# Kernel tuning notes

Hardware: AMD Instinct MI355X
Metric: run time of the kernel (lower is better)

Reference implementation:

```python
import jax, jax.numpy as jnp
import numpy as np

B, S, H = 64, 2048, 256
H3 = 3 * H


def setup_inputs() -> dict:
    key = jax.random.key(0)
    ks = jax.random.split(key, 5)
    static = jax.random.normal(ks[0], (B, S, H), dtype=jnp.float32)
    dynamic = jax.random.normal(ks[1], (B, S, H), dtype=jnp.float32)
    decoder_hidden = jax.random.normal(ks[2], (B, H), dtype=jnp.float32)
    # learned params (nn.Parameter in original); scale ~ 1/sqrt(fan_in)
    v = jax.random.normal(ks[3], (1, H3), dtype=jnp.float32) / np.sqrt(H3)
    W = jax.random.normal(ks[4], (H3, H3), dtype=jnp.float32) / np.sqrt(H3)
    return {"static": static, "dynamic": dynamic,
            "decoder_hidden": decoder_hidden, "v": v, "W": W}


def reference(static, dynamic, decoder_hidden, v, W):
    # cat = concat(static[i,j], dynamic[i,j], decoder_hidden[i]) -> [B, S, 3H]
    dec = jnp.broadcast_to(decoder_hidden[:, None, :], static.shape)
    cat = jnp.concatenate([static, dynamic, dec], axis=-1)
    # score[b,s] = v . tanh(W @ cat[b,s])
    hidden = jnp.tanh(jnp.einsum('ok,bsk->bso', W, cat))  # [B, S, 3H]
    scores = jnp.einsum('bso,o->bs', hidden, v[0])        # [B, S]
    return jax.nn.softmax(scores, axis=1)
```

## Files before the change

### kernel.cpp

```cpp
#include <hip/hip_runtime.h>
#include <hip/hip_bf16.h>

#define B_   64
#define S_   2048
#define H_   256
#define H3_  768
#define K_   512
#define MT   64
#define RSTR 1040

typedef __attribute__((ext_vector_type(8))) short  bf16x8;
typedef __attribute__((ext_vector_type(4))) float  f32x4;

__device__ __forceinline__ uint pkbf2(float a, float b) {
    float2 f = make_float2(a, b);
    __hip_bfloat162 h = __float22bfloat162_rn(f);
    return *reinterpret_cast<uint*>(&h);
}

__global__ void pack_w(const float* __restrict__ W, short* __restrict__ wpk) {
    int t = blockIdx.x * 256 + threadIdx.x;
    if (t >= 48 * 16 * 64) return;
    int lane = t & 63;
    int ks   = (t >> 6) & 15;
    int ot   = t >> 10;
    int o  = ot * 16 + (lane & 15);
    int kb = ks * 32 + (lane >> 4) * 8;
    const float* src = W + (size_t)o * H3_ + kb;
    float4 a = ((const float4*)src)[0];
    float4 b = ((const float4*)src)[1];
    uint4 pk;
    pk.x = pkbf2(a.x, a.y);
    pk.y = pkbf2(a.z, a.w);
    pk.z = pkbf2(b.x, b.y);
    pk.w = pkbf2(b.z, b.w);
    *(uint4*)(wpk + (size_t)t * 8) = pk;
}

__global__ void bias_k(const float* __restrict__ W, const float* __restrict__ dec,
                       const float* __restrict__ v, float* __restrict__ bias,
                       float* __restrict__ vsum) {
    if (blockIdx.x == 192) {
        if (threadIdx.x < 64) {
            float s = 0.f;
#pragma unroll
            for (int i = 0; i < 12; ++i) s += v[threadIdx.x + i * 64];
#pragma unroll
            for (int off = 32; off >= 1; off >>= 1) s += __shfl_xor(s, off);
            if (threadIdx.x == 0) vsum[0] = s;
        }
        return;
    }
    int idx = blockIdx.x * 256 + threadIdx.x;
    int b = idx / H3_;
    int o = idx - b * H3_;
    const float4* wr = (const float4*)(W + (size_t)o * H3_ + 2 * H_);
    const float4* dv = (const float4*)(dec + (size_t)b * H_);
    float s = 0.f;
#pragma unroll 8
    for (int k = 0; k < H_ / 4; ++k) {
        float4 a = wr[k], d = dv[k];
        s += a.x * d.x + a.y * d.y + a.z * d.z + a.w * d.w;
    }
    bias[idx] = s;
}

__global__ __launch_bounds__(512, 2)
void score_k(const float* __restrict__ stat, const float* __restrict__ dyn,
             const short* __restrict__ wpk, const float* __restrict__ bias,
             const float* __restrict__ v, const float* __restrict__ vsum,
             float* __restrict__ scores) {
    __shared__ char  aT[MT * RSTR];
    __shared__ float sred[8][MT];

    const int tid  = threadIdx.x;
    const int pos0 = blockIdx.x * MT;
    const int bidx = pos0 >> 11;

    const int wave = tid >> 6;
    const int lane = tid & 63;
    const int lr = lane & 15;
    const int lg = lane >> 4;

    const short* wbase = wpk + (size_t)lane * 8;

    bf16x8 bcur[3];
#pragma unroll
    for (int ni = 0; ni < 3; ++ni)
        bcur[ni] = *(const bf16x8*)(wbase + (size_t)(wave * 6 + ni) * 8192);

    {
        const int kcol = lane * 8;
        const float* srcbase = (kcol < 256) ? (stat + kcol) : (dyn + (kcol - 256));
#pragma unroll
        for (int bat = 0; bat < 2; ++bat) {
            float4 f0[4], f1[4];
#pragma unroll
            for (int u = 0; u < 4; ++u) {
                int row = (bat * 4 + u) * 8 + wave;
                const float4* p = (const float4*)(srcbase + (size_t)(pos0 + row) * H_);
                f0[u] = p[0];
                f1[u] = p[1];
            }
#pragma unroll
            for (int u = 0; u < 4; ++u) {
                int row = (bat * 4 + u) * 8 + wave;
                uint4 pk;
                pk.x = pkbf2(f0[u].x, f0[u].y);
                pk.y = pkbf2(f0[u].z, f0[u].w);
                pk.z = pkbf2(f1[u].x, f1[u].y);
                pk.w = pkbf2(f1[u].z, f1[u].w);
                *(uint4*)(aT + row * RSTR + lane * 16) = pk;
            }
        }
    }
    __syncthreads();

    const char* abase = aT + lr * RSTR + lg * 16;

    float sacc[4][4];
#pragma unroll
    for (int mi = 0; mi < 4; ++mi)
#pragma unroll
        for (int j = 0; j < 4; ++j) sacc[mi][j] = 0.f;

    const float C1 = 2.8853900817779268f;

#pragma unroll
    for (int p = 0; p < 2; ++p) {
        const int obase = wave * 96 + p * 48;

        float bv[3], vv2[3];
#pragma unroll
        for (int ni = 0; ni < 3; ++ni) {
            int o = obase + ni * 16 + lr;
            bv[ni]  = bias[bidx * H3_ + o];
            vv2[ni] = -2.0f * v[o];
        }

        f32x4 acc[4][3];
#pragma unroll
        for (int mi = 0; mi < 4; ++mi)
#pragma unroll
            for (int ni = 0; ni < 3; ++ni) {
                f32x4 a = {bv[ni], bv[ni], bv[ni], bv[ni]};
                acc[mi][ni] = a;
            }

        const short* wp0 = wbase + (size_t)(wave * 6 + p * 3) * 8192;

#pragma unroll 4
        for (int ks = 0; ks < 16; ++ks) {
            const int ksn = (ks + 1) & 15;
            bf16x8 bnx[3];
#pragma unroll
            for (int ni = 0; ni < 3; ++ni)
                bnx[ni] = *(const bf16x8*)(wp0 + ni * 8192 + ksn * 512);
            bf16x8 afr[4];
#pragma unroll
            for (int mi = 0; mi < 4; ++mi)
                afr[mi] = *(const bf16x8*)(abase + mi * 16 * RSTR + ks * 64);
            __builtin_amdgcn_s_setprio(1);
#pragma unroll
            for (int mi = 0; mi < 4; ++mi)
#pragma unroll
                for (int ni = 0; ni < 3; ++ni)
                    acc[mi][ni] = __builtin_amdgcn_mfma_f32_16x16x32_bf16(
                        afr[mi], bcur[ni], acc[mi][ni], 0, 0, 0);
            __builtin_amdgcn_s_setprio(0);
#pragma unroll
            for (int ni = 0; ni < 3; ++ni) bcur[ni] = bnx[ni];
        }

        if (p == 0) {
            const short* wpn = wbase + (size_t)(wave * 6 + 3) * 8192;
#pragma unroll
            for (int ni = 0; ni < 3; ++ni)
                bcur[ni] = *(const bf16x8*)(wpn + ni * 8192);
        }

#pragma unroll
        for (int ni = 0; ni < 3; ++ni)
#pragma unroll
            for (int mi = 0; mi < 4; ++mi)
#pragma unroll
                for (int j = 0; j < 4; ++j) {
                    float e = __builtin_amdgcn_exp2f(acc[mi][ni][j] * C1);
                    float r = __builtin_amdgcn_rcpf(e + 1.0f);
                    sacc[mi][j] = fmaf(vv2[ni], r, sacc[mi][j]);
                }
    }

#pragma unroll
    for (int mi = 0; mi < 4; ++mi)
#pragma unroll
        for (int j = 0; j < 4; ++j) {
            float x = sacc[mi][j];
            x += __shfl_xor(x, 1);
            x += __shfl_xor(x, 2);
            x += __shfl_xor(x, 4);
            x += __shfl_xor(x, 8);
            sacc[mi][j] = x;
        }
    if (lr == 0) {
#pragma unroll
        for (int mi = 0; mi < 4; ++mi)
#pragma unroll
            for (int j = 0; j < 4; ++j)
                sred[wave][mi * 16 + lg * 4 + j] = sacc[mi][j];
    }
    __syncthreads();
    if (tid < MT) {
        float s = vsum[0];
#pragma unroll
        for (int w = 0; w < 8; ++w) s += sred[w][tid];
        scores[pos0 + tid] = s;
    }
}

__global__ void softmax_k(float* __restrict__ out) {
    const int b = blockIdx.x;
    float* row = out + (size_t)b * S_;
    const int tid  = threadIdx.x;
    const int wave = tid >> 6;
    const int lane = tid & 63;

    float vals[8];
    float m = -1e30f;
#pragma unroll
    for (int i = 0; i < 8; ++i) {
        vals[i] = row[tid + i * 256];
        m = fmaxf(m, vals[i]);
    }
#pragma unroll
    for (int off = 32; off >= 1; off >>= 1) m = fmaxf(m, __shfl_xor(m, off));
    __shared__ float redm[4];
    __shared__ float reds[4];
    if (lane == 0) redm[wave] = m;
    __syncthreads();
    m = fmaxf(fmaxf(redm[0], redm[1]), fmaxf(redm[2], redm[3]));

    float s = 0.f;
#pragma unroll
    for (int i = 0; i < 8; ++i) {
        vals[i] = __expf(vals[i] - m);
        s += vals[i];
    }
#pragma unroll
    for (int off = 32; off >= 1; off >>= 1) s += __shfl_xor(s, off);
    if (lane == 0) reds[wave] = s;
    __syncthreads();
    s = reds[0] + reds[1] + reds[2] + reds[3];
    float inv = 1.0f / s;
#pragma unroll
    for (int i = 0; i < 8; ++i) row[tid + i * 256] = vals[i] * inv;
}

extern "C" void kernel_launch(void* const* d_in, const int* in_sizes, int n_in,
                              void* d_out, int out_size, void* d_ws, size_t ws_size,
                              hipStream_t stream) {
    const float* stat = (const float*)d_in[0];
    const float* dyn  = (const float*)d_in[1];
    const float* dec  = (const float*)d_in[2];
    const float* v    = (const float*)d_in[3];
    const float* W    = (const float*)d_in[4];
    float* out = (float*)d_out;

    short* wpk  = (short*)d_ws;
    float* bias = (float*)((char*)d_ws + (size_t)H3_ * K_ * 2);
    float* vsum = bias + B_ * H3_;

    pack_w <<<(48 * 16 * 64 + 255) / 256, 256, 0, stream>>>(W, wpk);
    bias_k <<<193, 256, 0, stream>>>(W, dec, v, bias, vsum);
    score_k<<<(B_ * S_) / MT, 512, 0, stream>>>(stat, dyn, wpk, bias, v, vsum, out);
    softmax_k<<<B_, 256, 0, stream>>>(out);
}
```

Measured before the change: 158.1 us.

## Split output columns across four blocks per tile with double-buffered K staging

Each 64-row tile is now processed by four 256-thread blocks, each owning a quarter of the output columns. Activations are staged in 128-column chunks into double-buffered LDS, so global loads overlap with MFMA work. Weights are loaded directly per k-step. Partial scores go to a workspace that softmax sums, and the constant v-sum term is dropped because softmax is shift-invariant. The change raises occupancy and overlap at the cost of reading each activation tile four times from global or L2 memory.

```diff
diff --git a/kernel.cpp b/kernel.cpp
--- a/kernel.cpp
+++ b/kernel.cpp
@@ -7,7 +7,7 @@
 #define H3_  768
 #define K_   512
 #define MT   64
-#define RSTR 1040
+#define RST  136
 
 typedef __attribute__((ext_vector_type(8))) short  bf16x8;
 typedef __attribute__((ext_vector_type(4))) float  f32x4;
@@ -38,20 +38,9 @@
 }
 
 __global__ void bias_k(const float* __restrict__ W, const float* __restrict__ dec,
-                       const float* __restrict__ v, float* __restrict__ bias,
-                       float* __restrict__ vsum) {
-    if (blockIdx.x == 192) {
-        if (threadIdx.x < 64) {
-            float s = 0.f;
-#pragma unroll
-            for (int i = 0; i < 12; ++i) s += v[threadIdx.x + i * 64];
-#pragma unroll
-            for (int off = 32; off >= 1; off >>= 1) s += __shfl_xor(s, off);
-            if (threadIdx.x == 0) vsum[0] = s;
-        }
-        return;
-    }
+                       float* __restrict__ bias) {
     int idx = blockIdx.x * 256 + threadIdx.x;
+    if (idx >= B_ * H3_) return;
     int b = idx / H3_;
     int o = idx - b * H3_;
     const float4* wr = (const float4*)(W + (size_t)o * H3_ + 2 * H_);
@@ -65,131 +54,119 @@
     bias[idx] = s;
 }
 
-__global__ __launch_bounds__(512, 2)
+__global__ __launch_bounds__(256, 4)
 void score_k(const float* __restrict__ stat, const float* __restrict__ dyn,
              const short* __restrict__ wpk, const float* __restrict__ bias,
-             const float* __restrict__ v, const float* __restrict__ vsum,
-             float* __restrict__ scores) {
-    __shared__ char  aT[MT * RSTR];
-    __shared__ float sred[8][MT];
+             const float* __restrict__ v, float* __restrict__ part) {
+    __shared__ short aT[2][MT * RST];
+    __shared__ float sred[4][MT];
 
     const int tid  = threadIdx.x;
-    const int pos0 = blockIdx.x * MT;
+    const int bid  = blockIdx.x;
+    const int rt   = bid >> 2;
+    const int g    = bid & 3;
+    const int pos0 = rt * MT;
     const int bidx = pos0 >> 11;
 
     const int wave = tid >> 6;
     const int lane = tid & 63;
-    const int lr = lane & 15;
-    const int lg = lane >> 4;
-
-    const short* wbase = wpk + (size_t)lane * 8;
-
-    bf16x8 bcur[3];
-#pragma unroll
-    for (int ni = 0; ni < 3; ++ni)
-        bcur[ni] = *(const bf16x8*)(wbase + (size_t)(wave * 6 + ni) * 8192);
-
-    {
-        const int kcol = lane * 8;
-        const float* srcbase = (kcol < 256) ? (stat + kcol) : (dyn + (kcol - 256));
-#pragma unroll
-        for (int bat = 0; bat < 2; ++bat) {
-            float4 f0[4], f1[4];
-#pragma unroll
-            for (int u = 0; u < 4; ++u) {
-                int row = (bat * 4 + u) * 8 + wave;
-                const float4* p = (const float4*)(srcbase + (size_t)(pos0 + row) * H_);
-                f0[u] = p[0];
-                f1[u] = p[1];
-            }
-#pragma unroll
-            for (int u = 0; u < 4; ++u) {
-                int row = (bat * 4 + u) * 8 + wave;
-                uint4 pk;
-                pk.x = pkbf2(f0[u].x, f0[u].y);
-                pk.y = pkbf2(f0[u].z, f0[u].w);
-                pk.z = pkbf2(f1[u].x, f1[u].y);
-                pk.w = pkbf2(f1[u].z, f1[u].w);
-                *(uint4*)(aT + row * RSTR + lane * 16) = pk;
-            }
-        }
-    }
-    __syncthreads();
-
-    const char* abase = aT + lr * RSTR + lg * 16;
-
-    float sacc[4][4];
+    const int lr   = lane & 15;
+    const int lg   = lane >> 4;
+
+    const float C1 = 2.8853900817779268f;
+
+    float bv[3], vv2[3];
+#pragma unroll
+    for (int ni = 0; ni < 3; ++ni) {
+        int o = (g * 12 + wave * 3 + ni) * 16 + lr;
+        bv[ni]  = bias[bidx * H3_ + o];
+        vv2[ni] = -2.0f * v[o];
+    }
+
+    const int srow = tid >> 2;
+    const int q    = tid & 3;
+    float4 f0[4], f1[4];
+    auto stage_load = [&](int ch) {
+        const float* base = (ch < 2)
+            ? (stat + (size_t)(pos0 + srow) * H_ + ch * 128 + q * 32)
+            : (dyn  + (size_t)(pos0 + srow) * H_ + (ch - 2) * 128 + q * 32);
+#pragma unroll
+        for (int u = 0; u < 4; ++u) {
+            f0[u] = ((const float4*)base)[u * 2];
+            f1[u] = ((const float4*)base)[u * 2 + 1];
+        }
+    };
+    auto stage_write = [&](int bufi) {
+        short* dst = aT[bufi] + srow * RST + q * 32;
+#pragma unroll
+        for (int u = 0; u < 4; ++u) {
+            uint4 pk;
+            pk.x = pkbf2(f0[u].x, f0[u].y);
+            pk.y = pkbf2(f0[u].z, f0[u].w);
+            pk.z = pkbf2(f1[u].x, f1[u].y);
+            pk.w = pkbf2(f1[u].z, f1[u].w);
+            *(uint4*)(dst + u * 8) = pk;
+        }
+    };
+
+    f32x4 acc[4][3];
 #pragma unroll
     for (int mi = 0; mi < 4; ++mi)
 #pragma unroll
-        for (int j = 0; j < 4; ++j) sacc[mi][j] = 0.f;
-
-    const float C1 = 2.8853900817779268f;
-
-#pragma unroll
-    for (int p = 0; p < 2; ++p) {
-        const int obase = wave * 96 + p * 48;
-
-        float bv[3], vv2[3];
-#pragma unroll
         for (int ni = 0; ni < 3; ++ni) {
-            int o = obase + ni * 16 + lr;
-            bv[ni]  = bias[bidx * H3_ + o];
-            vv2[ni] = -2.0f * v[o];
-        }
-
-        f32x4 acc[4][3];
-#pragma unroll
-        for (int mi = 0; mi < 4; ++mi)
-#pragma unroll
-            for (int ni = 0; ni < 3; ++ni) {
-                f32x4 a = {bv[ni], bv[ni], bv[ni], bv[ni]};
-                acc[mi][ni] = a;
-            }
-
-        const short* wp0 = wbase + (size_t)(wave * 6 + p * 3) * 8192;
-
-#pragma unroll 4
-        for (int ks = 0; ks < 16; ++ks) {
-            const int ksn = (ks + 1) & 15;
-            bf16x8 bnx[3];
+            f32x4 a = {bv[ni], bv[ni], bv[ni], bv[ni]};
+            acc[mi][ni] = a;
+        }
+
+    const short* wbase = wpk + (size_t)(g * 12 + wave * 3) * 8192 + lane * 8;
+
+    stage_load(0);
+    stage_write(0);
+    __syncthreads();
+
+#pragma unroll 1
+    for (int ch = 0; ch < 4; ++ch) {
+        if (ch < 3) stage_load(ch + 1);
+        const short* abuf = aT[ch & 1] + lr * RST + lg * 8;
+#pragma unroll
+        for (int ksl = 0; ksl < 4; ++ksl) {
+            const int ks = ch * 4 + ksl;
+            bf16x8 bfr[3];
 #pragma unroll
             for (int ni = 0; ni < 3; ++ni)
-                bnx[ni] = *(const bf16x8*)(wp0 + ni * 8192 + ksn * 512);
+                bfr[ni] = *(const bf16x8*)(wbase + ni * 8192 + ks * 512);
             bf16x8 afr[4];
 #pragma unroll
             for (int mi = 0; mi < 4; ++mi)
-                afr[mi] = *(const bf16x8*)(abase + mi * 16 * RSTR + ks * 64);
+                afr[mi] = *(const bf16x8*)(abuf + mi * 16 * RST + ksl * 32);
             __builtin_amdgcn_s_setprio(1);
 #pragma unroll
             for (int mi = 0; mi < 4; ++mi)
 #pragma unroll
                 for (int ni = 0; ni < 3; ++ni)
                     acc[mi][ni] = __builtin_amdgcn_mfma_f32_16x16x32_bf16(
-                        afr[mi], bcur[ni], acc[mi][ni], 0, 0, 0);
+                        afr[mi], bfr[ni], acc[mi][ni], 0, 0, 0);
             __builtin_amdgcn_s_setprio(0);
-#pragma unroll
-            for (int ni = 0; ni < 3; ++ni) bcur[ni] = bnx[ni];
-        }
-
-        if (p == 0) {
-            const short* wpn = wbase + (size_t)(wave * 6 + 3) * 8192;
-#pragma unroll
-            for (int ni = 0; ni < 3; ++ni)
-                bcur[ni] = *(const bf16x8*)(wpn + ni * 8192);
-        }
-
-#pragma unroll
-        for (int ni = 0; ni < 3; ++ni)
-#pragma unroll
-            for (int mi = 0; mi < 4; ++mi)
-#pragma unroll
-                for (int j = 0; j < 4; ++j) {
-                    float e = __builtin_amdgcn_exp2f(acc[mi][ni][j] * C1);
-                    float r = __builtin_amdgcn_rcpf(e + 1.0f);
-                    sacc[mi][j] = fmaf(vv2[ni], r, sacc[mi][j]);
-                }
-    }
+        }
+        if (ch < 3) stage_write((ch + 1) & 1);
+        __syncthreads();
+    }
+
+    float sacc[4][4];
+#pragma unroll
+    for (int mi = 0; mi < 4; ++mi)
+#pragma unroll
+        for (int j = 0; j < 4; ++j) sacc[mi][j] = 0.f;
+#pragma unroll
+    for (int ni = 0; ni < 3; ++ni)
+#pragma unroll
+        for (int mi = 0; mi < 4; ++mi)
+#pragma unroll
+            for (int j = 0; j < 4; ++j) {
+                float e = __builtin_amdgcn_exp2f(acc[mi][ni][j] * C1);
+                float r = __builtin_amdgcn_rcpf(e + 1.0f);
+                sacc[mi][j] = fmaf(vv2[ni], r, sacc[mi][j]);
+            }
 
 #pragma unroll
     for (int mi = 0; mi < 4; ++mi)
@@ -211,25 +188,25 @@
     }
     __syncthreads();
     if (tid < MT) {
-        float s = vsum[0];
-#pragma unroll
-        for (int w = 0; w < 8; ++w) s += sred[w][tid];
-        scores[pos0 + tid] = s;
-    }
-}
-
-__global__ void softmax_k(float* __restrict__ out) {
+        float s = sred[0][tid] + sred[1][tid] + sred[2][tid] + sred[3][tid];
+        part[(size_t)g * (B_ * S_) + pos0 + tid] = s;
+    }
+}
+
+__global__ void softmax_k(const float* __restrict__ part, float* __restrict__ out) {
     const int b = blockIdx.x;
-    float* row = out + (size_t)b * S_;
     const int tid  = threadIdx.x;
     const int wave = tid >> 6;
     const int lane = tid & 63;
+    const int base = b * S_;
 
     float vals[8];
     float m = -1e30f;
 #pragma unroll
     for (int i = 0; i < 8; ++i) {
-        vals[i] = row[tid + i * 256];
+        int idx = base + tid + i * 256;
+        vals[i] = part[idx] + part[idx + B_ * S_] + part[idx + 2 * B_ * S_]
+                + part[idx + 3 * B_ * S_];
         m = fmaxf(m, vals[i]);
     }
 #pragma unroll
@@ -252,6 +229,7 @@
     __syncthreads();
     s = reds[0] + reds[1] + reds[2] + reds[3];
     float inv = 1.0f / s;
+    float* row = out + (size_t)base;
 #pragma unroll
     for (int i = 0; i < 8; ++i) row[tid + i * 256] = vals[i] * inv;
 }
@@ -268,10 +246,10 @@
 
     short* wpk  = (short*)d_ws;
     float* bias = (float*)((char*)d_ws + (size_t)H3_ * K_ * 2);
-    float* vsum = bias + B_ * H3_;
+    float* part = bias + B_ * H3_;
 
     pack_w <<<(48 * 16 * 64 + 255) / 256, 256, 0, stream>>>(W, wpk);
-    bias_k <<<193, 256, 0, stream>>>(W, dec, v, bias, vsum);
-    score_k<<<(B_ * S_) / MT, 512, 0, stream>>>(stat, dyn, wpk, bias, v, vsum, out);
-    softmax_k<<<B_, 256, 0, stream>>>(out);
-}
+    bias_k <<<(B_ * H3_ + 255) / 256, 256, 0, stream>>>(W, dec, bias);
+    score_k<<<(B_ * S_ / MT) * 4, 256, 0, stream>>>(stat, dyn, wpk, bias, v, part);
+    softmax_k<<<B_, 256, 0, stream>>>(part, out);
+}
```

Result: slower. 590.5 us (+273.4%).

## Double M tile to 128 rows and overlap dynamic-half loads with MFMA

Applied to the files above, without the earlier changes.

The score kernel tile grows from 64 to 128 positions per block, so each weight fragment loaded from global memory feeds twice as many MFMAs. The static and dynamic halves of the activation tile are staged separately, and the dynamic half's global loads and bf16 packing are interleaved with the first eight k-steps of the first output pass, hiding part of the load latency. The softmax-invariant vsum constant is dropped, and launch bounds fall to one block per SM. The larger register and LDS footprint lowers occupancy and spills could hurt.

```diff
diff --git a/kernel.cpp b/kernel.cpp
--- a/kernel.cpp
+++ b/kernel.cpp
@@ -5,9 +5,9 @@
 #define S_   2048
 #define H_   256
 #define H3_  768
-#define K_   512
-#define MT   64
-#define RSTR 1040
+#define MT   128
+#define RSH  528
+#define HALF (MT * RSH)
 
 typedef __attribute__((ext_vector_type(8))) short  bf16x8;
 typedef __attribute__((ext_vector_type(4))) float  f32x4;
@@ -38,20 +38,9 @@
 }
 
 __global__ void bias_k(const float* __restrict__ W, const float* __restrict__ dec,
-                       const float* __restrict__ v, float* __restrict__ bias,
-                       float* __restrict__ vsum) {
-    if (blockIdx.x == 192) {
-        if (threadIdx.x < 64) {
-            float s = 0.f;
-#pragma unroll
-            for (int i = 0; i < 12; ++i) s += v[threadIdx.x + i * 64];
-#pragma unroll
-            for (int off = 32; off >= 1; off >>= 1) s += __shfl_xor(s, off);
-            if (threadIdx.x == 0) vsum[0] = s;
-        }
-        return;
-    }
+                       float* __restrict__ bias) {
     int idx = blockIdx.x * 256 + threadIdx.x;
+    if (idx >= B_ * H3_) return;
     int b = idx / H3_;
     int o = idx - b * H3_;
     const float4* wr = (const float4*)(W + (size_t)o * H3_ + 2 * H_);
@@ -65,12 +54,11 @@
     bias[idx] = s;
 }
 
-__global__ __launch_bounds__(512, 2)
+__global__ __launch_bounds__(512, 1)
 void score_k(const float* __restrict__ stat, const float* __restrict__ dyn,
              const short* __restrict__ wpk, const float* __restrict__ bias,
-             const float* __restrict__ v, const float* __restrict__ vsum,
-             float* __restrict__ scores) {
-    __shared__ char  aT[MT * RSTR];
+             const float* __restrict__ v, float* __restrict__ scores) {
+    __shared__ char  aT[2 * HALF];
     __shared__ float sred[8][MT];
 
     const int tid  = threadIdx.x;
@@ -79,110 +67,120 @@
 
     const int wave = tid >> 6;
     const int lane = tid & 63;
-    const int lr = lane & 15;
-    const int lg = lane >> 4;
-
+    const int lr   = lane & 15;
+    const int lg   = lane >> 4;
+
+    const float C1 = 2.8853900817779268f;
     const short* wbase = wpk + (size_t)lane * 8;
 
+    float4 f0[4], f1[4];
+    auto loadb = [&](int h, int bat) {
+        const float* srcb = (h == 0) ? stat : dyn;
+#pragma unroll
+        for (int i = 0; i < 4; ++i) {
+            int lin = (bat * 4 + i) * 512 + tid;
+            int row = lin >> 5;
+            int un  = lin & 31;
+            const float4* p = (const float4*)(srcb + (size_t)(pos0 + row) * H_ + un * 8);
+            f0[i] = p[0];
+            f1[i] = p[1];
+        }
+    };
+    auto writeb = [&](int h, int bat) {
+#pragma unroll
+        for (int i = 0; i < 4; ++i) {
+            int lin = (bat * 4 + i) * 512 + tid;
+            int row = lin >> 5;
+            int un  = lin & 31;
+            uint4 pk;
+            pk.x = pkbf2(f0[i].x, f0[i].y);
+            pk.y = pkbf2(f0[i].z, f0[i].w);
+            pk.z = pkbf2(f1[i].x, f1[i].y);
+            pk.w = pkbf2(f1[i].z, f1[i].w);
+            *(uint4*)(aT + h * HALF + row * RSH + un * 16) = pk;
+        }
+    };
+
+    loadb(0, 0); writeb(0, 0);
+    loadb(0, 1); writeb(0, 1);
+    __syncthreads();
+
+    float sacc[8][4];
+#pragma unroll
+    for (int mi = 0; mi < 8; ++mi)
+#pragma unroll
+        for (int j = 0; j < 4; ++j) sacc[mi][j] = 0.f;
+
+    const char* abase0 = aT + lr * RSH + lg * 16;
+
+    f32x4 acc[8][3];
     bf16x8 bcur[3];
-#pragma unroll
-    for (int ni = 0; ni < 3; ++ni)
-        bcur[ni] = *(const bf16x8*)(wbase + (size_t)(wave * 6 + ni) * 8192);
+    auto ksstep = [&](const short* wp, int ks) {
+        const int h = ks >> 3, ksl = ks & 7;
+        const int ksn = (ks + 1) & 15;
+        bf16x8 bnx[3];
+#pragma unroll
+        for (int ni = 0; ni < 3; ++ni)
+            bnx[ni] = *(const bf16x8*)(wp + ni * 8192 + ksn * 512);
+        const char* ab = abase0 + h * HALF + ksl * 64;
+        bf16x8 afr[8];
+#pragma unroll
+        for (int mi = 0; mi < 8; ++mi)
+            afr[mi] = *(const bf16x8*)(ab + mi * (16 * RSH));
+        __builtin_amdgcn_s_setprio(1);
+#pragma unroll
+        for (int mi = 0; mi < 8; ++mi)
+#pragma unroll
+            for (int ni = 0; ni < 3; ++ni)
+                acc[mi][ni] = __builtin_amdgcn_mfma_f32_16x16x32_bf16(
+                    afr[mi], bcur[ni], acc[mi][ni], 0, 0, 0);
+        __builtin_amdgcn_s_setprio(0);
+#pragma unroll
+        for (int ni = 0; ni < 3; ++ni) bcur[ni] = bnx[ni];
+    };
+
+    const short* wp0 = wbase + (size_t)(wave * 6) * 8192;
+    const short* wp1 = wbase + (size_t)(wave * 6 + 3) * 8192;
 
     {
-        const int kcol = lane * 8;
-        const float* srcbase = (kcol < 256) ? (stat + kcol) : (dyn + (kcol - 256));
-#pragma unroll
-        for (int bat = 0; bat < 2; ++bat) {
-            float4 f0[4], f1[4];
-#pragma unroll
-            for (int u = 0; u < 4; ++u) {
-                int row = (bat * 4 + u) * 8 + wave;
-                const float4* p = (const float4*)(srcbase + (size_t)(pos0 + row) * H_);
-                f0[u] = p[0];
-                f1[u] = p[1];
-            }
-#pragma unroll
-            for (int u = 0; u < 4; ++u) {
-                int row = (bat * 4 + u) * 8 + wave;
-                uint4 pk;
-                pk.x = pkbf2(f0[u].x, f0[u].y);
-                pk.y = pkbf2(f0[u].z, f0[u].w);
-                pk.z = pkbf2(f1[u].x, f1[u].y);
-                pk.w = pkbf2(f1[u].z, f1[u].w);
-                *(uint4*)(aT + row * RSTR + lane * 16) = pk;
-            }
-        }
-    }
-    __syncthreads();
-
-    const char* abase = aT + lr * RSTR + lg * 16;
-
-    float sacc[4][4];
-#pragma unroll
-    for (int mi = 0; mi < 4; ++mi)
-#pragma unroll
-        for (int j = 0; j < 4; ++j) sacc[mi][j] = 0.f;
-
-    const float C1 = 2.8853900817779268f;
-
-#pragma unroll
-    for (int p = 0; p < 2; ++p) {
-        const int obase = wave * 96 + p * 48;
-
         float bv[3], vv2[3];
 #pragma unroll
         for (int ni = 0; ni < 3; ++ni) {
-            int o = obase + ni * 16 + lr;
+            int o = (wave * 6 + ni) * 16 + lr;
             bv[ni]  = bias[bidx * H3_ + o];
             vv2[ni] = -2.0f * v[o];
         }
-
-        f32x4 acc[4][3];
-#pragma unroll
-        for (int mi = 0; mi < 4; ++mi)
+#pragma unroll
+        for (int mi = 0; mi < 8; ++mi)
 #pragma unroll
             for (int ni = 0; ni < 3; ++ni) {
                 f32x4 a = {bv[ni], bv[ni], bv[ni], bv[ni]};
                 acc[mi][ni] = a;
             }
-
-        const short* wp0 = wbase + (size_t)(wave * 6 + p * 3) * 8192;
-
+#pragma unroll
+        for (int ni = 0; ni < 3; ++ni)
+            bcur[ni] = *(const bf16x8*)(wp0 + ni * 8192);
+
+        loadb(1, 0);
 #pragma unroll 4
-        for (int ks = 0; ks < 16; ++ks) {
-            const int ksn = (ks + 1) & 15;
-            bf16x8 bnx[3];
-#pragma unroll
-            for (int ni = 0; ni < 3; ++ni)
-                bnx[ni] = *(const bf16x8*)(wp0 + ni * 8192 + ksn * 512);
-            bf16x8 afr[4];
-#pragma unroll
-            for (int mi = 0; mi < 4; ++mi)
-                afr[mi] = *(const bf16x8*)(abase + mi * 16 * RSTR + ks * 64);
-            __builtin_amdgcn_s_setprio(1);
-#pragma unroll
-            for (int mi = 0; mi < 4; ++mi)
-#pragma unroll
-                for (int ni = 0; ni < 3; ++ni)
-                    acc[mi][ni] = __builtin_amdgcn_mfma_f32_16x16x32_bf16(
-                        afr[mi], bcur[ni], acc[mi][ni], 0, 0, 0);
-            __builtin_amdgcn_s_setprio(0);
-#pragma unroll
-            for (int ni = 0; ni < 3; ++ni) bcur[ni] = bnx[ni];
-        }
-
-        if (p == 0) {
-            const short* wpn = wbase + (size_t)(wave * 6 + 3) * 8192;
-#pragma unroll
-            for (int ni = 0; ni < 3; ++ni)
-                bcur[ni] = *(const bf16x8*)(wpn + ni * 8192);
-        }
-
-#pragma unroll
-        for (int ni = 0; ni < 3; ++ni)
-#pragma unroll
-            for (int mi = 0; mi < 4; ++mi)
+        for (int ks = 0; ks < 4; ++ks) ksstep(wp0, ks);
+        writeb(1, 0);
+        loadb(1, 1);
+#pragma unroll 4
+        for (int ks = 4; ks < 8; ++ks) ksstep(wp0, ks);
+        writeb(1, 1);
+        __syncthreads();
+#pragma unroll 4
+        for (int ks = 8; ks < 16; ++ks) ksstep(wp0, ks);
+
+#pragma unroll
+        for (int ni = 0; ni < 3; ++ni)
+            bcur[ni] = *(const bf16x8*)(wp1 + ni * 8192);
+
+#pragma unroll
+        for (int ni = 0; ni < 3; ++ni)
+#pragma unroll
+            for (int mi = 0; mi < 8; ++mi)
 #pragma unroll
                 for (int j = 0; j < 4; ++j) {
                     float e = __builtin_amdgcn_exp2f(acc[mi][ni][j] * C1);
@@ -191,8 +189,38 @@
                 }
     }
 
-#pragma unroll
-    for (int mi = 0; mi < 4; ++mi)
+    {
+        float bv[3], vv2[3];
+#pragma unroll
+        for (int ni = 0; ni < 3; ++ni) {
+            int o = (wave * 6 + 3 + ni) * 16 + lr;
+            bv[ni]  = bias[bidx * H3_ + o];
+            vv2[ni] = -2.0f * v[o];
+        }
+#pragma unroll
+        for (int mi = 0; mi < 8; ++mi)
+#pragma unroll
+            for (int ni = 0; ni < 3; ++ni) {
+                f32x4 a = {bv[ni], bv[ni], bv[ni], bv[ni]};
+                acc[mi][ni] = a;
+            }
+#pragma unroll 4
+        for (int ks = 0; ks < 16; ++ks) ksstep(wp1, ks);
+
+#pragma unroll
+        for (int ni = 0; ni < 3; ++ni)
+#pragma unroll
+            for (int mi = 0; mi < 8; ++mi)
+#pragma unroll
+                for (int j = 0; j < 4; ++j) {
+                    float e = __builtin_amdgcn_exp2f(acc[mi][ni][j] * C1);
+                    float r = __builtin_amdgcn_rcpf(e + 1.0f);
+                    sacc[mi][j] = fmaf(vv2[ni], r, sacc[mi][j]);
+                }
+    }
+
+#pragma unroll
+    for (int mi = 0; mi < 8; ++mi)
 #pragma unroll
         for (int j = 0; j < 4; ++j) {
             float x = sacc[mi][j];
@@ -204,14 +232,14 @@
         }
     if (lr == 0) {
 #pragma unroll
-        for (int mi = 0; mi < 4; ++mi)
+        for (int mi = 0; mi < 8; ++mi)
 #pragma unroll
             for (int j = 0; j < 4; ++j)
                 sred[wave][mi * 16 + lg * 4 + j] = sacc[mi][j];
     }
     __syncthreads();
     if (tid < MT) {
-        float s = vsum[0];
+        float s = 0.f;
 #pragma unroll
         for (int w = 0; w < 8; ++w) s += sred[w][tid];
         scores[pos0 + tid] = s;
@@ -267,11 +295,10 @@
     float* out = (float*)d_out;
 
     short* wpk  = (short*)d_ws;
-    float* bias = (float*)((char*)d_ws + (size_t)H3_ * K_ * 2);
-    float* vsum = bias + B_ * H3_;
+    float* bias = (float*)((char*)d_ws + (size_t)H3_ * 512 * 2);
 
     pack_w <<<(48 * 16 * 64 + 255) / 256, 256, 0, stream>>>(W, wpk);
-    bias_k <<<193, 256, 0, stream>>>(W, dec, v, bias, vsum);
-    score_k<<<(B_ * S_) / MT, 512, 0, stream>>>(stat, dyn, wpk, bias, v, vsum, out);
+    bias_k <<<(B_ * H3_ + 255) / 256, 256, 0, stream>>>(W, dec, bias);
+    score_k<<<(B_ * S_) / MT, 512, 0, stream>>>(stat, dyn, wpk, bias, v, out);
     softmax_k<<<B_, 256, 0, stream>>>(out);
 }
```

After: 152.6 us. 1.04x faster.
